# Kernel optimization log

Measured on AMD Instinct MI355X. Metric: run time of the kernel, lower is better.

## Reference

```python
import jax, jax.numpy as jnp
import numpy as np

K = 50          # NEC paper uses p=50 neighbors
DELTA = 1e-3    # kernel smoothing constant


def setup_inputs() -> dict:
    key = jax.random.key(0)
    ks = jax.random.split(key, 8)
    B, D_IN, D, A, C = 512, 2, 128, 3, 200000
    s = lambda fan_in: 1.0 / np.sqrt(fan_in)
    return {
        "x": jax.random.normal(ks[0], (B, D_IN), jnp.float32),
        "W1": jax.random.normal(ks[1], (D_IN, D), jnp.float32) * s(D_IN),
        "b1": jnp.zeros((D,), jnp.float32),
        "W2": jax.random.normal(ks[2], (D, D), jnp.float32) * s(D),
        "b2": jnp.zeros((D,), jnp.float32),
        "W3": jax.random.normal(ks[3], (D, D), jnp.float32) * s(D),
        "b3": jnp.zeros((D,), jnp.float32),
        "W4": jax.random.normal(ks[4], (D, D), jnp.float32) * s(D),
        "b4": jnp.zeros((D,), jnp.float32),
        "keys": jax.random.normal(ks[5], (A, C, D), jnp.float32),
        "mem_values": jax.random.normal(ks[6], (A, C), jnp.float32),
    }


def _encode(x, W1, b1, W2, b2, W3, b3, W4, b4):
    h = jax.nn.relu(x @ W1 + b1)
    h = jax.nn.relu(h @ W2 + b2)
    h = jax.nn.relu(h @ W3 + b3)
    return h @ W4 + b4  # [B, D]


def _dnd_lookup(h, keys, mem_values):
    # h: [B, D]; keys: [A, C, D]; mem_values: [A, C]
    q2 = jnp.sum(h * h, axis=-1)                       # [B]
    k2 = jnp.sum(keys * keys, axis=-1)                 # [A, C]
    cross = jnp.einsum("bd,acd->bac", h, keys)         # [B, A, C]
    d2 = jnp.maximum(q2[:, None, None] + k2[None] - 2.0 * cross, 0.0)
    neg_d, idx = jax.lax.top_k(-d2, K)                  # [B, A, K]
    d_top = -neg_d
    w = 1.0 / (d_top + DELTA)                           # NEC kernel
    w = w / jnp.sum(w, axis=-1, keepdims=True)
    a_idx = jnp.arange(keys.shape[0])[None, :, None]    # [1, A, 1]
    v_top = mem_values[a_idx, idx]                      # gather -> [B, A, K]
    values = jnp.sum(w * v_top, axis=-1)                # [B, A]
    return values


def reference(x, W1, b1, W2, b2, W3, b3, W4, b4, keys, mem_values):
    h = _encode(x, W1, b1, W2, b2, W3, b3, W4, b4)
    values = _dnd_lookup(h, keys, mem_values)
    actions = jnp.argmax(values, axis=-1)
    return values, actions
```

## Files before the change

### kernel.cpp

```cpp
#include <hip/hip_runtime.h>
#include <hip/hip_bf16.h>
#include <math.h>

#define B_    512
#define DIM   128
#define A_    3
#define C_    200000
#define K_    50
#define DELTA 1e-3

typedef __attribute__((ext_vector_type(8))) short bf16x8;
typedef __attribute__((ext_vector_type(4))) float f32x4;

#define NBIN_A 128
#define CAP_A  1024
#define NSEG_G 128
#define TPS_G  13
#define NT_G   1563
#define HSEG   16
#define CHPS   782
#define ROWCH  12500

#define AOFF_H64   0u
#define AOFF_H32   524288u
#define AOFF_HBF   786432u
#define AOFF_Q2    917504u
#define AOFF_HIST  919552u
#define AOFF_CNT   1705984u
#define AOFF_TAUB  1712128u
#define AOFF_V64   1718272u
#define AOFF_CAND  1730560u
#define AOFF_BINS  8022016u
#define NEED_A     (8022016ull + 307200000ull)

#define NBIN_B 192
#define CAP_B  768
#define BM_B   64
#define BN_B   128
#define TPC_B  16
#define CHUNK_B (TPC_B*BN_B)
#define NCH_B  ((C_ + CHUNK_B - 1)/CHUNK_B)

#define BOFF_H32   0u
#define BOFF_H64   262144u
#define BOFF_Q2    786432u
#define BOFF_K2    788480u
#define BOFF_HIST  3188480u
#define BOFF_TAU   4368128u
#define BOFF_CNT   4374272u
#define BOFF_V64   4380416u
#define BOFF_CAND  4392704u

static __device__ inline unsigned short f2bf(float x) {
    union { float f; unsigned u; } c; c.f = x;
    unsigned r = (c.u + 0x7FFFu + ((c.u >> 16) & 1u)) >> 16;
    return (unsigned short)r;
}
static __device__ inline unsigned pkbf(float a, float b) {
    __hip_bfloat162 t = __float22bfloat162_rn(make_float2(a, b));
    union { __hip_bfloat162 h; unsigned u; } cv; cv.h = t; return cv.u;
}

__global__ __launch_bounds__(128) void mlp_kernel(
    const float* __restrict__ x,
    const float* __restrict__ W1, const float* __restrict__ b1,
    const float* __restrict__ W2, const float* __restrict__ b2,
    const float* __restrict__ W3, const float* __restrict__ b3,
    const float* __restrict__ W4, const float* __restrict__ b4,
    float* __restrict__ h32, unsigned short* __restrict__ hbf,
    double* __restrict__ h64, float* __restrict__ q2)
{
    int b = blockIdx.x, t = threadIdx.x;
    __shared__ double s0[DIM], s1[DIM];
    double x0 = (double)x[b*2+0], x1 = (double)x[b*2+1];
    double h = x0*(double)W1[t] + x1*(double)W1[DIM+t] + (double)b1[t];
    s0[t] = h > 0.0 ? h : 0.0;
    __syncthreads();
    double acc = (double)b2[t];
    for (int k = 0; k < DIM; k++) acc += s0[k]*(double)W2[k*DIM+t];
    s1[t] = acc > 0.0 ? acc : 0.0;
    __syncthreads();
    acc = (double)b3[t];
    for (int k = 0; k < DIM; k++) acc += s1[k]*(double)W3[k*DIM+t];
    s0[t] = acc > 0.0 ? acc : 0.0;
    __syncthreads();
    acc = (double)b4[t];
    for (int k = 0; k < DIM; k++) acc += s0[k]*(double)W4[k*DIM+t];
    h64[b*DIM+t] = acc;
    float hf = (float)acc;
    h32[b*DIM+t] = hf;
    hbf[b*DIM+t] = f2bf(hf);
    s1[t] = acc*acc;
    __syncthreads();
    for (int s = 64; s > 0; s >>= 1) { if (t < s) s1[t] += s1[t+s]; __syncthreads(); }
    if (t == 0) q2[b] = (float)s1[0];
}

__global__ __launch_bounds__(256, 2) void gemm_bin_kernel(
    const float* __restrict__ keys, const unsigned short* __restrict__ hbf,
    const float* __restrict__ q2, unsigned char* __restrict__ bins)
{
    const int seg = blockIdx.x, my = blockIdx.y, a = blockIdx.z;
    const int b0 = my*128;
    const int tid = threadIdx.x;
    const int lane = tid & 63, w = tid >> 6;
    const int lm = lane & 15, kh = lane >> 4;
    const int wm = w & 1, wn = w >> 1;

    __shared__ short sA[128*136];
    __shared__ short sB[128*136];
    __shared__ float q2s[128];
    __shared__ float k2s[128];

    {
        int r = tid >> 1, hh = tid & 1;
        const int4* gp = (const int4*)hbf + (size_t)(b0 + r)*16 + hh*8;
        int4* dp = (int4*)&sA[r*136 + hh*64];
        #pragma unroll
        for (int q = 0; q < 8; q++) dp[q] = gp[q];
        if (tid < 128) q2s[tid] = q2[b0 + tid];
    }

    for (int t = 0; t < TPS_G; t++) {
        int nt = seg*TPS_G + t;
        if (nt >= NT_G) break;
        int n0 = nt*128;
        __syncthreads();
        {
            int r = tid >> 1, hh = tid & 1;
            int nr = n0 + r; if (nr >= C_) nr = C_-1;
            const float4* gp = (const float4*)(keys + ((size_t)a*C_ + nr)*128) + hh*16;
            float ss = 0.0f;
            int4* dp = (int4*)&sB[r*136 + hh*64];
            #pragma unroll
            for (int q = 0; q < 8; q++) {
                float4 v0 = gp[2*q], v1 = gp[2*q+1];
                ss += v0.x*v0.x + v0.y*v0.y + v0.z*v0.z + v0.w*v0.w
                    + v1.x*v1.x + v1.y*v1.y + v1.z*v1.z + v1.w*v1.w;
                int4 pk;
                pk.x = (int)pkbf(v0.x, v0.y);
                pk.y = (int)pkbf(v0.z, v0.w);
                pk.z = (int)pkbf(v1.x, v1.y);
                pk.w = (int)pkbf(v1.z, v1.w);
                dp[q] = pk;
            }
            ss += __shfl_xor(ss, 1, 64);
            if (hh == 0) k2s[r] = ss;
        }
        __syncthreads();

        f32x4 acc[4][4];
        #pragma unroll
        for (int i = 0; i < 4; i++)
            #pragma unroll
            for (int j = 0; j < 4; j++) acc[i][j] = (f32x4){0.f, 0.f, 0.f, 0.f};

        #pragma unroll
        for (int kst = 0; kst < 4; kst++) {
            bf16x8 af[4], bfv[4];
            #pragma unroll
            for (int i = 0; i < 4; i++)
                af[i] = *(const bf16x8*)&sA[(wm*64 + i*16 + lm)*136 + kst*32 + kh*8];
            #pragma unroll
            for (int j = 0; j < 4; j++)
                bfv[j] = *(const bf16x8*)&sB[(wn*64 + j*16 + lm)*136 + kst*32 + kh*8];
            #pragma unroll
            for (int i = 0; i < 4; i++)
                #pragma unroll
                for (int j = 0; j < 4; j++)
                    acc[i][j] = __builtin_amdgcn_mfma_f32_16x16x32_bf16(af[i], bfv[j], acc[i][j], 0, 0, 0);
        }

        unsigned char* bp = bins + ((size_t)(a*B_ + b0))*C_ + n0;
        #pragma unroll
        for (int j = 0; j < 4; j++) {
            int col = wn*64 + j*16 + lm;
            int n = n0 + col;
            if (n < C_) {
                float kk = k2s[col];
                #pragma unroll
                for (int i = 0; i < 4; i++) {
                    int rl = wm*64 + i*16 + kh*4;
                    #pragma unroll
                    for (int reg = 0; reg < 4; reg++) {
                        float d2v = q2s[rl+reg] + kk - 2.0f*acc[i][j][reg];
                        float dc = fminf(fmaxf(d2v, 16.0f), 4095.0f);
                        int bin = (int)(__float_as_uint(dc) >> 19) - 2096;
                        bp[(size_t)(rl+reg)*C_ + col] = (unsigned char)bin;
                    }
                }
            }
        }
    }
}

__global__ __launch_bounds__(256) void histA_kernel(const unsigned char* __restrict__ bins,
                                                    unsigned* __restrict__ hist)
{
    int q = blockIdx.x;
    int seg = blockIdx.y;
    int tid = threadIdx.x;
    int a = q >> 9, b = q & 511;
    int p = b*A_ + a;
    __shared__ unsigned hs[NBIN_A*8];
    for (int i = tid; i < NBIN_A*8; i += 256) hs[i] = 0;
    __syncthreads();
    const uint4* row = (const uint4*)(bins + (size_t)q*C_);
    int ch0 = seg*CHPS, ch1 = ch0 + CHPS; if (ch1 > ROWCH) ch1 = ROWCH;
    int rep = tid & 7;
    for (int ch = ch0 + tid; ch < ch1; ch += 256) {
        uint4 v = row[ch];
        unsigned d[4] = {v.x, v.y, v.z, v.w};
        #pragma unroll
        for (int e = 0; e < 4; e++) {
            unsigned x = d[e];
            atomicAdd(&hs[((x      ) & 127u)*8 + rep], 1u);
            atomicAdd(&hs[((x >>  8) & 127u)*8 + rep], 1u);
            atomicAdd(&hs[((x >> 16) & 127u)*8 + rep], 1u);
            atomicAdd(&hs[((x >> 24) & 127u)*8 + rep], 1u);
        }
    }
    __syncthreads();
    if (tid < NBIN_A) {
        unsigned s = 0;
        #pragma unroll
        for (int r2 = 0; r2 < 8; r2++) s += hs[tid*8 + r2];
        if (s) atomicAdd(&hist[(size_t)p*NBIN_A + tid], s);
    }
}

__global__ void tauA_kernel(const unsigned* __restrict__ hist, int* __restrict__ taubin)
{
    int p = blockIdx.x*256 + threadIdx.x;
    if (p >= B_*A_) return;
    const unsigned* hp = hist + (size_t)p*NBIN_A;
    unsigned cum = 0; int jsel = NBIN_A-1;
    for (int j = 0; j < NBIN_A; j++) { cum += hp[j]; if (cum >= K_) { jsel = j; break; } }
    unsigned c1 = cum + (jsel+1 < NBIN_A ? hp[jsel+1] : 0u);
    unsigned c2 = c1  + (jsel+2 < NBIN_A ? hp[jsel+2] : 0u);
    int jt = (c2 <= 768u) ? jsel+2 : jsel+1;
    if (jt > NBIN_A-1) jt = NBIN_A-1;
    taubin[p] = jt;
}

__global__ __launch_bounds__(256) void collectA_kernel(const unsigned char* __restrict__ bins,
    const int* __restrict__ taubin, unsigned* __restrict__ cnt, int* __restrict__ cand)
{
    int q = blockIdx.x, seg = blockIdx.y, tid = threadIdx.x;
    int a = q >> 9, b = q & 511;
    int p = b*A_ + a;
    int tb = taubin[p];
    unsigned thr  = (unsigned)(tb + 1);
    unsigned addv = (128u - thr) * 0x01010101u;
    const uint4* row = (const uint4*)(bins + (size_t)q*C_);
    int ch0 = seg*CHPS, ch1 = ch0 + CHPS; if (ch1 > ROWCH) ch1 = ROWCH;
    for (int ch = ch0 + tid; ch < ch1; ch += 256) {
        uint4 v = row[ch];
        unsigned d[4] = {v.x, v.y, v.z, v.w};
        #pragma unroll
        for (int e = 0; e < 4; e++) {
            unsigned m = (d[e] + addv) & 0x80808080u;
            if (m != 0x80808080u) {
                #pragma unroll
                for (int by = 0; by < 4; by++) {
                    if (!((m >> (8*by + 7)) & 1u)) {
                        int n = ch*16 + e*4 + by;
                        unsigned pos = atomicAdd(&cnt[p], 1u);
                        if (pos < CAP_A) cand[(size_t)p*CAP_A + pos] = n;
                    }
                }
            }
        }
    }
}

__global__ __launch_bounds__(256) void k2_kernel(const float* __restrict__ keys,
                                                 float* __restrict__ k2)
{
    int r = blockIdx.x*4 + (threadIdx.x >> 6);
    int lane = threadIdx.x & 63;
    float2 v = ((const float2*)keys)[(size_t)r*64 + lane];
    float s = v.x*v.x + v.y*v.y;
    #pragma unroll
    for (int off = 32; off > 0; off >>= 1) s += __shfl_down(s, off, 64);
    if (lane == 0) k2[r] = s;
}

template<int MODE>
__global__ __launch_bounds__(256) void pass_kernel(
    const float* __restrict__ keys, const float* __restrict__ h32,
    const float* __restrict__ q2,   const float* __restrict__ k2,
    unsigned* __restrict__ hist,    const float* __restrict__ tau,
    unsigned* __restrict__ cnt,     int* __restrict__ cand)
{
    const int bt = blockIdx.x;
    const int ch = blockIdx.y;
    const int a  = blockIdx.z;
    const int b0 = bt*BM_B;
    const int tid = threadIdx.x;
    const int tx = tid & 31, ty = tid >> 5;

    __shared__ float4 hs4[BM_B*33];
    __shared__ float4 ks4[BN_B*33];
    __shared__ float  q2s[BM_B];
    __shared__ float  taus[BM_B];
    __shared__ unsigned hist_s[MODE == 0 ? BM_B*NBIN_B : 1];

    #pragma unroll
    for (int q = 0; q < BM_B*32/256; q++) {
        int flat = q*256 + tid; int row = flat >> 5, kq = flat & 31;
        hs4[row*33 + kq] = ((const float4*)h32)[(size_t)(b0+row)*32 + kq];
    }
    if (tid < BM_B) {
        q2s[tid] = q2[b0+tid];
        if (MODE == 1) taus[tid] = tau[(b0+tid)*A_ + a];
    }
    if (MODE == 0) for (int i = tid; i < BM_B*NBIN_B; i += 256) hist_s[i] = 0;
    const float* __restrict__ k2g = k2 + (size_t)a*C_;

    for (int t = 0; t < TPC_B; t++) {
        int n0 = ch*CHUNK_B + t*BN_B;
        if (n0 >= C_) break;
        __syncthreads();
        #pragma unroll
        for (int q = 0; q < 16; q++) {
            int flat = q*256 + tid; int row = flat >> 5, kq = flat & 31;
            int nr = n0 + row; if (nr >= C_) nr = C_-1;
            ks4[row*33 + kq] = ((const float4*)keys)[((size_t)a*C_ + nr)*32 + kq];
        }
        __syncthreads();

        float acc[8][4];
        #pragma unroll
        for (int i = 0; i < 8; i++)
            #pragma unroll
            for (int j = 0; j < 4; j++) acc[i][j] = 0.0f;

        for (int kq = 0; kq < 32; kq++) {
            float4 hv[8], kv[4];
            #pragma unroll
            for (int i = 0; i < 8; i++) hv[i] = hs4[(ty*8+i)*33 + kq];
            #pragma unroll
            for (int j = 0; j < 4; j++) kv[j] = ks4[(j*32+tx)*33 + kq];
            #pragma unroll
            for (int i = 0; i < 8; i++)
                #pragma unroll
                for (int j = 0; j < 4; j++)
                    acc[i][j] += hv[i].x*kv[j].x + hv[i].y*kv[j].y
                               + hv[i].z*kv[j].z + hv[i].w*kv[j].w;
        }

        #pragma unroll
        for (int i = 0; i < 8; i++) {
            int bl = ty*8 + i;
            float q2b = q2s[bl];
            #pragma unroll
            for (int j = 0; j < 4; j++) {
                int n = n0 + j*32 + tx;
                if (n < C_) {
                    float d2f = fmaxf(q2b + k2g[n] - 2.0f*acc[i][j], 0.0f);
                    if (MODE == 0) {
                        int bin = (int)(__float_as_uint(d2f + 1.0f) >> 19) - 2032;
                        bin = bin < 0 ? 0 : (bin > NBIN_B-1 ? NBIN_B-1 : bin);
                        atomicAdd(&hist_s[bl*NBIN_B + bin], 1u);
                    } else {
                        if (d2f < taus[bl]) {
                            int p = (b0+bl)*A_ + a;
                            unsigned pos = atomicAdd(&cnt[p], 1u);
                            if (pos < CAP_B) cand[(size_t)p*CAP_B + pos] = n;
                        }
                    }
                }
            }
        }
    }
    if (MODE == 0) {
        __syncthreads();
        for (int i = tid; i < BM_B*NBIN_B; i += 256) {
            unsigned v = hist_s[i];
            if (v) {
                int bl = i / NBIN_B, bin = i % NBIN_B;
                atomicAdd(&hist[(size_t)((b0+bl)*A_ + a)*NBIN_B + bin], v);
            }
        }
    }
}

__global__ __launch_bounds__(256) void tauB_kernel(const unsigned* __restrict__ hist,
                                                   float* __restrict__ tau)
{
    int p = blockIdx.x*256 + threadIdx.x;
    if (p >= B_*A_) return;
    const unsigned* hp = hist + (size_t)p*NBIN_B;
    unsigned cum = 0; int jsel = NBIN_B-1;
    for (int j = 0; j < NBIN_B; j++) { cum += hp[j]; if (cum >= K_) { jsel = j; break; } }
    tau[p] = __uint_as_float((unsigned)(2034 + jsel) << 19) - 1.0f;
}

__global__ __launch_bounds__(256) void select_kernel(
    const float* __restrict__ keys, const double* __restrict__ h64,
    const float* __restrict__ mem_values,
    const unsigned* __restrict__ cnt, const int* __restrict__ cand,
    float* __restrict__ out_values, double* __restrict__ val64, int cap)
{
    int p = blockIdx.x; int b = p / A_, a = p % A_;
    int tid = threadIdx.x;
    __shared__ double hd[DIM];
    __shared__ double d2s[CAP_A];
    __shared__ float  vs[CAP_A];
    __shared__ double red[256];
    __shared__ int    redi[256];
    __shared__ double acc_w, acc_wv;

    for (int i = tid; i < DIM; i += 256) hd[i] = h64[(size_t)b*DIM + i];
    if (tid == 0) { acc_w = 0.0; acc_wv = 0.0; }
    __syncthreads();

    int n = (int)cnt[p]; if (n > cap) n = cap;
    for (int i = tid; i < n; i += 256) {
        int c = cand[(size_t)p*cap + i];
        const float4* kr = (const float4*)(keys + ((size_t)a*C_ + c)*DIM);
        double s0 = 0.0, s1 = 0.0;
        #pragma unroll 4
        for (int kq = 0; kq < 32; kq++) {
            float4 kv = kr[kq];
            double d0 = hd[4*kq+0] - (double)kv.x;
            double d1 = hd[4*kq+1] - (double)kv.y;
            double d2 = hd[4*kq+2] - (double)kv.z;
            double d3 = hd[4*kq+3] - (double)kv.w;
            s0 += d0*d0 + d1*d1; s1 += d2*d2 + d3*d3;
        }
        d2s[i] = s0 + s1;
        vs[i]  = mem_values[(size_t)a*C_ + c];
    }
    __syncthreads();

    int kk = n < K_ ? n : K_;
    for (int t = 0; t < kk; t++) {
        double best = 1e300; int bi = -1;
        for (int i = tid; i < n; i += 256)
            if (d2s[i] < best) { best = d2s[i]; bi = i; }
        red[tid] = best; redi[tid] = bi;
        __syncthreads();
        for (int s = 128; s > 0; s >>= 1) {
            if (tid < s && red[tid+s] < red[tid]) { red[tid] = red[tid+s]; redi[tid] = redi[tid+s]; }
            __syncthreads();
        }
        if (tid == 0) {
            int wi = redi[0];
            double d = d2s[wi]; if (d < 0.0) d = 0.0;
            double wgt = 1.0 / (d + DELTA);
            acc_w += wgt; acc_wv += wgt * (double)vs[wi];
            d2s[wi] = 2e300;
        }
        __syncthreads();
    }
    if (tid == 0) {
        double v = acc_wv / acc_w;
        out_values[p] = (float)v;
        val64[p] = v;
    }
}

__global__ void argmax_kernel(const double* __restrict__ val64, float* __restrict__ out)
{
    int b = blockIdx.x*blockDim.x + threadIdx.x;
    if (b >= B_) return;
    double v0 = val64[b*A_+0], v1 = val64[b*A_+1], v2 = val64[b*A_+2];
    int bi = 0; double bv = v0;
    if (v1 > bv) { bv = v1; bi = 1; }
    if (v2 > bv) { bv = v2; bi = 2; }
    out[B_*A_ + b] = (float)bi;
}

extern "C" void kernel_launch(void* const* d_in, const int* in_sizes, int n_in,
                              void* d_out, int out_size, void* d_ws, size_t ws_size,
                              hipStream_t stream)
{
    const float* x    = (const float*)d_in[0];
    const float* W1   = (const float*)d_in[1];
    const float* b1   = (const float*)d_in[2];
    const float* W2   = (const float*)d_in[3];
    const float* b2   = (const float*)d_in[4];
    const float* W3   = (const float*)d_in[5];
    const float* b3   = (const float*)d_in[6];
    const float* W4   = (const float*)d_in[7];
    const float* b4   = (const float*)d_in[8];
    const float* keys = (const float*)d_in[9];
    const float* memv = (const float*)d_in[10];

    char* ws = (char*)d_ws;

    if (ws_size >= NEED_A) {
        double*         h64  = (double*)        (ws + AOFF_H64);
        float*          h32  = (float*)         (ws + AOFF_H32);
        unsigned short* hbf  = (unsigned short*)(ws + AOFF_HBF);
        float*          q2   = (float*)         (ws + AOFF_Q2);
        unsigned*       hist = (unsigned*)      (ws + AOFF_HIST);
        unsigned*       cnt  = (unsigned*)      (ws + AOFF_CNT);
        int*            taub = (int*)           (ws + AOFF_TAUB);
        double*         v64  = (double*)        (ws + AOFF_V64);
        int*            cand = (int*)           (ws + AOFF_CAND);
        unsigned char*  bins = (unsigned char*) (ws + AOFF_BINS);

        hipMemsetAsync(ws + AOFF_HIST, 0, (AOFF_CNT + B_*A_*4) - AOFF_HIST, stream);

        mlp_kernel<<<B_, 128, 0, stream>>>(x, W1, b1, W2, b2, W3, b3, W4, b4, h32, hbf, h64, q2);
        gemm_bin_kernel<<<dim3(NSEG_G, 4, A_), 256, 0, stream>>>(keys, hbf, q2, bins);
        histA_kernel<<<dim3(B_*A_, HSEG), 256, 0, stream>>>(bins, hist);
        tauA_kernel<<<(B_*A_ + 255)/256, 256, 0, stream>>>(hist, taub);
        collectA_kernel<<<dim3(B_*A_, HSEG), 256, 0, stream>>>(bins, taub, cnt, cand);
        select_kernel<<<B_*A_, 256, 0, stream>>>(keys, h64, memv, cnt, cand, (float*)d_out, v64, CAP_A);
        argmax_kernel<<<2, 256, 0, stream>>>(v64, (float*)d_out);
    } else {
        float*          h32  = (float*)         (ws + BOFF_H32);
        double*         h64  = (double*)        (ws + BOFF_H64);
        float*          q2   = (float*)         (ws + BOFF_Q2);
        float*          k2   = (float*)         (ws + BOFF_K2);
        unsigned*       hist = (unsigned*)      (ws + BOFF_HIST);
        float*          tau  = (float*)         (ws + BOFF_TAU);
        unsigned*       cnt  = (unsigned*)      (ws + BOFF_CNT);
        double*         v64  = (double*)        (ws + BOFF_V64);
        int*            cand = (int*)           (ws + BOFF_CAND);
        unsigned short* hbf  = (unsigned short*)(ws + BOFF_CAND);

        hipMemsetAsync(ws + BOFF_HIST, 0, (BOFF_CNT + B_*A_*4) - BOFF_HIST, stream);

        mlp_kernel<<<B_, 128, 0, stream>>>(x, W1, b1, W2, b2, W3, b3, W4, b4, h32, hbf, h64, q2);
        k2_kernel<<<(A_*C_)/4, 256, 0, stream>>>(keys, k2);
        pass_kernel<0><<<dim3(B_/BM_B, NCH_B, A_), 256, 0, stream>>>(keys, h32, q2, k2, hist, nullptr, nullptr, nullptr);
        tauB_kernel<<<(B_*A_ + 255)/256, 256, 0, stream>>>(hist, tau);
        pass_kernel<1><<<dim3(B_/BM_B, NCH_B, A_), 256, 0, stream>>>(keys, h32, q2, k2, nullptr, tau, cnt, cand);
        select_kernel<<<B_*A_, 256, 0, stream>>>(keys, h64, memv, cnt, cand, (float*)d_out, v64, CAP_B);
        argmax_kernel<<<2, 256, 0, stream>>>(v64, (float*)d_out);
    }
}
```

Before: 1.061 ms.

## Pack bin writes as 32-bit words and use single-wavefront register top-K select

```diff
diff --git a/kernel.cpp b/kernel.cpp
--- a/kernel.cpp
+++ b/kernel.cpp
@@ -20,6 +20,7 @@
 #define HSEG   16
 #define CHPS   782
 #define ROWCH  12500
+#define NL     16
 
 #define AOFF_H64   0u
 #define AOFF_H32   524288u
@@ -105,17 +106,18 @@
     const int tid = threadIdx.x;
     const int lane = tid & 63, w = tid >> 6;
     const int lm = lane & 15, kh = lane >> 4;
-    const int wm = w & 1, wn = w >> 1;
+    const int wm = w & 1;
+    const int wn = w >> 1;
 
     __shared__ short sA[128*136];
     __shared__ short sB[128*136];
-    __shared__ float q2s[128];
-    __shared__ float k2s[128];
+    __shared__ __align__(16) float q2s[128];
+    __shared__ __align__(16) float k2s[128];
 
     {
         int r = tid >> 1, hh = tid & 1;
         const int4* gp = (const int4*)hbf + (size_t)(b0 + r)*16 + hh*8;
-        int4* dp = (int4*)&sA[r*136 + hh*64];
+        int4* dp = (int4*)&sB[r*136 + hh*64];
         #pragma unroll
         for (int q = 0; q < 8; q++) dp[q] = gp[q];
         if (tid < 128) q2s[tid] = q2[b0 + tid];
@@ -131,7 +133,7 @@
             int nr = n0 + r; if (nr >= C_) nr = C_-1;
             const float4* gp = (const float4*)(keys + ((size_t)a*C_ + nr)*128) + hh*16;
             float ss = 0.0f;
-            int4* dp = (int4*)&sB[r*136 + hh*64];
+            int4* dp = (int4*)&sA[r*136 + hh*64];
             #pragma unroll
             for (int q = 0; q < 8; q++) {
                 float4 v0 = gp[2*q], v1 = gp[2*q+1];
@@ -171,23 +173,28 @@
                     acc[i][j] = __builtin_amdgcn_mfma_f32_16x16x32_bf16(af[i], bfv[j], acc[i][j], 0, 0, 0);
         }
 
-        unsigned char* bp = bins + ((size_t)(a*B_ + b0))*C_ + n0;
-        #pragma unroll
-        for (int j = 0; j < 4; j++) {
-            int col = wn*64 + j*16 + lm;
-            int n = n0 + col;
+        float qv[4];
+        #pragma unroll
+        for (int j = 0; j < 4; j++) qv[j] = q2s[wn*64 + j*16 + lm];
+        #pragma unroll
+        for (int i = 0; i < 4; i++) {
+            int nb = wm*64 + i*16 + kh*4;
+            int n  = n0 + nb;
+            float4 kb = *(const float4*)&k2s[nb];
             if (n < C_) {
-                float kk = k2s[col];
                 #pragma unroll
-                for (int i = 0; i < 4; i++) {
-                    int rl = wm*64 + i*16 + kh*4;
+                for (int j = 0; j < 4; j++) {
+                    int bl = wn*64 + j*16 + lm;
+                    unsigned pk = 0;
                     #pragma unroll
-                    for (int reg = 0; reg < 4; reg++) {
-                        float d2v = q2s[rl+reg] + kk - 2.0f*acc[i][j][reg];
-                        float dc = fminf(fmaxf(d2v, 16.0f), 4095.0f);
-                        int bin = (int)(__float_as_uint(dc) >> 19) - 2096;
-                        bp[(size_t)(rl+reg)*C_ + col] = (unsigned char)bin;
+                    for (int r = 0; r < 4; r++) {
+                        float kr = (r==0 ? kb.x : r==1 ? kb.y : r==2 ? kb.z : kb.w);
+                        float d2v = fmaf(-2.0f, acc[i][j][r], qv[j] + kr);
+                        float dc  = fminf(fmaxf(d2v, 16.0f), 4095.0f);
+                        unsigned u = (__float_as_uint(dc) >> 19) - 2096u;
+                        pk |= u << (8*r);
                     }
+                    *(unsigned*)(bins + ((size_t)(a*B_ + b0 + bl))*C_ + n) = pk;
                 }
             }
         }
@@ -272,6 +279,89 @@
             }
         }
     }
+}
+
+__global__ __launch_bounds__(64) void select_kernel(
+    const float* __restrict__ keys, const double* __restrict__ h64,
+    const float* __restrict__ mem_values,
+    const unsigned* __restrict__ cnt, const int* __restrict__ cand,
+    float* __restrict__ out_values, double* __restrict__ val64, int cap)
+{
+    int p = blockIdx.x; int b = p / A_, a = p % A_;
+    int lane = threadIdx.x;
+    __shared__ double hd[DIM];
+    __shared__ float  vsm[CAP_A];
+
+    for (int i = lane; i < DIM; i += 64) hd[i] = h64[(size_t)b*DIM + i];
+    int n = (int)cnt[p]; if (n > cap) n = cap;
+    __syncthreads();
+
+    double d2r[NL];
+    #pragma unroll
+    for (int s = 0; s < NL; s++) d2r[s] = 1e300;
+
+    #pragma unroll 1
+    for (int s = 0; s < NL; s++) {
+        int i = s*64 + lane;
+        if (i < n) {
+            int c = cand[(size_t)p*cap + i];
+            const float4* kr = (const float4*)(keys + ((size_t)a*C_ + c)*DIM);
+            double s0 = 0.0, s1 = 0.0;
+            #pragma unroll 4
+            for (int kq = 0; kq < 32; kq++) {
+                float4 kv = kr[kq];
+                double d0 = hd[4*kq+0] - (double)kv.x;
+                double d1 = hd[4*kq+1] - (double)kv.y;
+                double d2 = hd[4*kq+2] - (double)kv.z;
+                double d3 = hd[4*kq+3] - (double)kv.w;
+                s0 += d0*d0 + d1*d1; s1 += d2*d2 + d3*d3;
+            }
+            double d = s0 + s1;
+            unsigned long long bits = __double_as_longlong(d);
+            bits = (bits & ~1023ull) | (unsigned long long)i;
+            d2r[s] = __longlong_as_double(bits);
+            vsm[i] = mem_values[(size_t)a*C_ + c];
+        }
+    }
+    __syncthreads();
+
+    double accw = 0.0, accwv = 0.0;
+    for (int t = 0; t < K_; t++) {
+        double best = d2r[0];
+        #pragma unroll
+        for (int s = 1; s < NL; s++) best = fmin(best, d2r[s]);
+        #pragma unroll
+        for (int off = 32; off > 0; off >>= 1) {
+            double o = __shfl_xor(best, off, 64);
+            best = fmin(best, o);
+        }
+        if (best >= 1e300) break;
+        unsigned gidx = (unsigned)(__double_as_longlong(best) & 1023ull);
+        int ol = gidx & 63, os = gidx >> 6;
+        if (lane == ol) {
+            #pragma unroll
+            for (int s = 0; s < NL; s++) if (s == os) d2r[s] = 1e300;
+        }
+        double d = best; if (d < 0.0) d = 0.0;
+        double wgt = 1.0 / (d + DELTA);
+        accw += wgt; accwv += wgt * (double)vsm[gidx];
+    }
+    if (lane == 0) {
+        double v = accwv / accw;
+        out_values[p] = (float)v;
+        val64[p] = v;
+    }
+}
+
+__global__ void argmax_kernel(const double* __restrict__ val64, float* __restrict__ out)
+{
+    int b = blockIdx.x*blockDim.x + threadIdx.x;
+    if (b >= B_) return;
+    double v0 = val64[b*A_+0], v1 = val64[b*A_+1], v2 = val64[b*A_+2];
+    int bi = 0; double bv = v0;
+    if (v1 > bv) { bv = v1; bi = 1; }
+    if (v2 > bv) { bv = v2; bi = 2; }
+    out[B_*A_ + b] = (float)bi;
 }
 
 __global__ __launch_bounds__(256) void k2_kernel(const float* __restrict__ keys,
@@ -397,82 +487,6 @@
     tau[p] = __uint_as_float((unsigned)(2034 + jsel) << 19) - 1.0f;
 }
 
-__global__ __launch_bounds__(256) void select_kernel(
-    const float* __restrict__ keys, const double* __restrict__ h64,
-    const float* __restrict__ mem_values,
-    const unsigned* __restrict__ cnt, const int* __restrict__ cand,
-    float* __restrict__ out_values, double* __restrict__ val64, int cap)
-{
-    int p = blockIdx.x; int b = p / A_, a = p % A_;
-    int tid = threadIdx.x;
-    __shared__ double hd[DIM];
-    __shared__ double d2s[CAP_A];
-    __shared__ float  vs[CAP_A];
-    __shared__ double red[256];
-    __shared__ int    redi[256];
-    __shared__ double acc_w, acc_wv;
-
-    for (int i = tid; i < DIM; i += 256) hd[i] = h64[(size_t)b*DIM + i];
-    if (tid == 0) { acc_w = 0.0; acc_wv = 0.0; }
-    __syncthreads();
-
-    int n = (int)cnt[p]; if (n > cap) n = cap;
-    for (int i = tid; i < n; i += 256) {
-        int c = cand[(size_t)p*cap + i];
-        const float4* kr = (const float4*)(keys + ((size_t)a*C_ + c)*DIM);
-        double s0 = 0.0, s1 = 0.0;
-        #pragma unroll 4
-        for (int kq = 0; kq < 32; kq++) {
-            float4 kv = kr[kq];
-            double d0 = hd[4*kq+0] - (double)kv.x;
-            double d1 = hd[4*kq+1] - (double)kv.y;
-            double d2 = hd[4*kq+2] - (double)kv.z;
-            double d3 = hd[4*kq+3] - (double)kv.w;
-            s0 += d0*d0 + d1*d1; s1 += d2*d2 + d3*d3;
-        }
-        d2s[i] = s0 + s1;
-        vs[i]  = mem_values[(size_t)a*C_ + c];
-    }
-    __syncthreads();
-
-    int kk = n < K_ ? n : K_;
-    for (int t = 0; t < kk; t++) {
-        double best = 1e300; int bi = -1;
-        for (int i = tid; i < n; i += 256)
-            if (d2s[i] < best) { best = d2s[i]; bi = i; }
-        red[tid] = best; redi[tid] = bi;
-        __syncthreads();
-        for (int s = 128; s > 0; s >>= 1) {
-            if (tid < s && red[tid+s] < red[tid]) { red[tid] = red[tid+s]; redi[tid] = redi[tid+s]; }
-            __syncthreads();
-        }
-        if (tid == 0) {
-            int wi = redi[0];
-            double d = d2s[wi]; if (d < 0.0) d = 0.0;
-            double wgt = 1.0 / (d + DELTA);
-            acc_w += wgt; acc_wv += wgt * (double)vs[wi];
-            d2s[wi] = 2e300;
-        }
-        __syncthreads();
-    }
-    if (tid == 0) {
-        double v = acc_wv / acc_w;
-        out_values[p] = (float)v;
-        val64[p] = v;
-    }
-}
-
-__global__ void argmax_kernel(const double* __restrict__ val64, float* __restrict__ out)
-{
-    int b = blockIdx.x*blockDim.x + threadIdx.x;
-    if (b >= B_) return;
-    double v0 = val64[b*A_+0], v1 = val64[b*A_+1], v2 = val64[b*A_+2];
-    int bi = 0; double bv = v0;
-    if (v1 > bv) { bv = v1; bi = 1; }
-    if (v2 > bv) { bv = v2; bi = 2; }
-    out[B_*A_ + b] = (float)bi;
-}
-
 extern "C" void kernel_launch(void* const* d_in, const int* in_sizes, int n_in,
                               void* d_out, int out_size, void* d_ws, size_t ws_size,
                               hipStream_t stream)
@@ -510,7 +524,7 @@
         histA_kernel<<<dim3(B_*A_, HSEG), 256, 0, stream>>>(bins, hist);
         tauA_kernel<<<(B_*A_ + 255)/256, 256, 0, stream>>>(hist, taub);
         collectA_kernel<<<dim3(B_*A_, HSEG), 256, 0, stream>>>(bins, taub, cnt, cand);
-        select_kernel<<<B_*A_, 256, 0, stream>>>(keys, h64, memv, cnt, cand, (float*)d_out, v64, CAP_A);
+        select_kernel<<<B_*A_, 64, 0, stream>>>(keys, h64, memv, cnt, cand, (float*)d_out, v64, CAP_A);
         argmax_kernel<<<2, 256, 0, stream>>>(v64, (float*)d_out);
     } else {
         float*          h32  = (float*)         (ws + BOFF_H32);
@@ -531,7 +545,7 @@
         pass_kernel<0><<<dim3(B_/BM_B, NCH_B, A_), 256, 0, stream>>>(keys, h32, q2, k2, hist, nullptr, nullptr, nullptr);
         tauB_kernel<<<(B_*A_ + 255)/256, 256, 0, stream>>>(hist, tau);
         pass_kernel<1><<<dim3(B_/BM_B, NCH_B, A_), 256, 0, stream>>>(keys, h32, q2, k2, nullptr, tau, cnt, cand);
-        select_kernel<<<B_*A_, 256, 0, stream>>>(keys, h64, memv, cnt, cand, (float*)d_out, v64, CAP_B);
+        select_kernel<<<B_*A_, 64, 0, stream>>>(keys, h64, memv, cnt, cand, (float*)d_out, v64, CAP_B);
         argmax_kernel<<<2, 256, 0, stream>>>(v64, (float*)d_out);
     }
 }
```

New measurement: 1.098 ms. +3.5%, slower.
